# Optimization experiments

Hardware: AMD Instinct MI355X
Metric: run time of the kernel (lower is better)

## Reference

```python
import jax, jax.numpy as jnp
import numpy as np

MASK_VALUE = 0.0  # default `mask=0` scalar in the original forward


def setup_inputs() -> dict:
    key = jax.random.key(0)
    kq, kk, kv = jax.random.split(key, 3)
    b, n, d_k, d_v = 8, 2048, 64, 64
    q = jax.random.normal(kq, (b, n, d_k), dtype=jnp.float32)
    k = jax.random.normal(kk, (b, n, d_k), dtype=jnp.float32)
    v = jax.random.normal(kv, (b, n, d_v), dtype=jnp.float32)
    return {"q": q, "k": k, "v": v}


def reference(q, k, v):
    d_k = q.shape[-1]
    temper = jnp.asarray(d_k, q.dtype) ** 0.5
    # scores: (b, n, n)
    attn = jnp.einsum('bqd,bkd->bqk', q, k) / temper
    # equality-based masking: positions whose score exactly equals the
    # scalar `mask` (default 0) are set to -inf before softmax.
    attn = jnp.where(attn == MASK_VALUE, -jnp.inf, attn)
    # NOTE: the original code calls `attn.masked_fill(look_ahead_mask==0, -inf)`
    # WITHOUT assignment, so the look-ahead mask is a no-op; we omit it faithfully.
    attn = jax.nn.softmax(attn, axis=-1)
    out = jnp.einsum('bqk,bkd->bqd', attn, v)  # (b, n, d_v)
    return out
```

## Files before the change

### kernel.cpp

```cpp
#include <hip/hip_runtime.h>
#include <hip/hip_bf16.h>

typedef __bf16 bf16_t;
typedef bf16_t bf16x2 __attribute__((ext_vector_type(2)));
typedef bf16_t bf16x4 __attribute__((ext_vector_type(4)));
typedef bf16_t bf16x8 __attribute__((ext_vector_type(8)));
typedef float  floatx4  __attribute__((ext_vector_type(4)));
typedef float  floatx16 __attribute__((ext_vector_type(16)));

constexpr int B = 8, N = 2048, D = 64;
constexpr int KSTR = 72;
constexpr int VSTR = 136;
constexpr int TSTR = 65;

__global__ __launch_bounds__(256)
void prepass_kernel(const float* __restrict__ k, const float* __restrict__ v,
                    bf16_t* __restrict__ kb, bf16_t* __restrict__ vt) {
    __shared__ float t[64 * TSTR];
    const int tid = threadIdx.x;
    const int r0  = blockIdx.x * 64;
    const int b   = blockIdx.y;
    if (blockIdx.z == 0) {
        const float* src = k + ((size_t)b * N + r0) * D;
        bf16_t* dst = kb + ((size_t)b * N + r0) * D;
        #pragma unroll
        for (int p = 0; p < 4; ++p) {
            int e = (tid + p * 256) * 4;
            floatx4 f = *(const floatx4*)(src + e);
            bf16x4 o;
            #pragma unroll
            for (int j = 0; j < 4; ++j) o[j] = (bf16_t)f[j];
            *(bf16x4*)(dst + e) = o;
        }
    } else {
        const float* vb = v + ((size_t)b * N + r0) * D;
        #pragma unroll
        for (int p = 0; p < 4; ++p) {
            int e = (tid + p * 256) * 4;
            int row = e >> 6, col = e & 63;
            floatx4 f = *(const floatx4*)(vb + e);
            #pragma unroll
            for (int j = 0; j < 4; ++j) t[(col + j) * TSTR + row] = f[j];
        }
        __syncthreads();
        bf16_t* ob = vt + (size_t)b * D * N + r0;
        #pragma unroll
        for (int p = 0; p < 4; ++p) {
            int e = (tid + p * 256) * 4;
            int drow = e >> 6, kcol = e & 63;
            bf16x4 o;
            #pragma unroll
            for (int j = 0; j < 4; ++j) o[j] = (bf16_t)t[drow * TSTR + kcol + j];
            *(bf16x4*)(ob + (size_t)drow * N + kcol) = o;
        }
    }
}

__global__ __launch_bounds__(256, 4)
void attn_kernel(const float* __restrict__ q, const bf16_t* __restrict__ kb,
                 const bf16_t* __restrict__ vt, float* __restrict__ out) {
    __shared__ bf16_t lds_k[128 * KSTR];
    __shared__ bf16_t lds_v[64 * VSTR];
    __shared__ float  l_buf[3][32];
    float* o_buf = (float*)lds_k;

    const int tid  = threadIdx.x;
    const int lane = tid & 63;
    const int cg   = tid >> 6;
    const int h    = lane >> 5;
    const int l31  = lane & 31;

    const int b  = blockIdx.y;
    const int q0 = blockIdx.x * 32;

    const bf16_t* kbb = kb + (size_t)b * N * D;
    const bf16_t* vbb = vt + (size_t)b * D * N;

    bf16x8 qf[4];
    {
        const float* qp = q + ((size_t)b * N + q0 + l31) * D + h * 8;
        #pragma unroll
        for (int kd = 0; kd < 4; ++kd) {
            floatx4 f0 = *(const floatx4*)(qp + kd * 16);
            floatx4 f1 = *(const floatx4*)(qp + kd * 16 + 4);
            bf16x8 t;
            #pragma unroll
            for (int j = 0; j < 4; ++j) { t[j] = (bf16_t)f0[j]; t[j + 4] = (bf16_t)f1[j]; }
            qf[kd] = t;
        }
    }

    floatx16 o_acc[2];
    #pragma unroll
    for (int d = 0; d < 2; ++d)
        #pragma unroll
        for (int i = 0; i < 16; ++i) o_acc[d][i] = 0.f;
    float l_run = 0.f;

    bf16x8 kreg[4], vreg[4];
    #pragma unroll
    for (int p = 0; p < 4; ++p) {
        int e = (tid + p * 256) * 8;
        kreg[p] = *(const bf16x8*)(kbb + e);
        vreg[p] = *(const bf16x8*)(vbb + (size_t)(e >> 7) * N + (e & 127));
    }

    #pragma unroll 1
    for (int it = 0; it < N / 128; ++it) {
        __syncthreads();
        #pragma unroll
        for (int p = 0; p < 4; ++p) {
            int e = (tid + p * 256) * 8;
            *(bf16x8*)&lds_k[(e >> 6) * KSTR + (e & 63)] = kreg[p];
            *(bf16x8*)&lds_v[(e >> 7) * VSTR + (e & 127)] = vreg[p];
        }
        __syncthreads();
        if (it + 1 < N / 128) {
            const int kv1 = (it + 1) * 128;
            #pragma unroll
            for (int p = 0; p < 4; ++p) {
                int e = (tid + p * 256) * 8;
                kreg[p] = *(const bf16x8*)(kbb + (size_t)kv1 * D + e);
                vreg[p] = *(const bf16x8*)(vbb + (size_t)(e >> 7) * N + kv1 + (e & 127));
            }
        }

        floatx16 s;
        #pragma unroll
        for (int i = 0; i < 16; ++i) s[i] = 0.f;
        #pragma unroll
        for (int kd = 0; kd < 4; ++kd) {
            bf16x8 kf = *(const bf16x8*)&lds_k[(cg * 32 + l31) * KSTR + kd * 16 + h * 8];
            s = __builtin_amdgcn_mfma_f32_32x32x16_bf16(kf, qf[kd], s, 0, 0, 0);
        }

        int q8[8];
        #pragma unroll
        for (int g = 0; g < 8; ++g) {
            union { int i; bf16x2 h2; } u;
            #pragma unroll
            for (int j = 0; j < 2; ++j) {
                float x = s[2 * g + j] * 0.125f;
                float p = (x == 0.0f) ? 0.0f : __expf(x);
                l_run += p;
                u.h2[j] = (bf16_t)p;
            }
            q8[g] = u.i;
        }

        #pragma unroll
        for (int s2 = 0; s2 < 2; ++s2) {
            int r0 = __shfl_xor(q8[4 * s2 + 0], 32);
            int r1 = __shfl_xor(q8[4 * s2 + 1], 32);
            int r2 = __shfl_xor(q8[4 * s2 + 2], 32);
            int r3 = __shfl_xor(q8[4 * s2 + 3], 32);
            union { int i4[4]; bf16x8 v; } bf;
            bf.i4[0] = h ? r2 : q8[4 * s2 + 0];
            bf.i4[1] = h ? r3 : q8[4 * s2 + 1];
            bf.i4[2] = h ? q8[4 * s2 + 2] : r0;
            bf.i4[3] = h ? q8[4 * s2 + 3] : r1;
            #pragma unroll
            for (int dblk = 0; dblk < 2; ++dblk) {
                bf16x8 va = *(const bf16x8*)&lds_v[(dblk * 32 + l31) * VSTR + cg * 32 + s2 * 16 + h * 8];
                o_acc[dblk] = __builtin_amdgcn_mfma_f32_32x32x16_bf16(va, bf.v, o_acc[dblk], 0, 0, 0);
            }
        }
    }

    __syncthreads();

    l_run += __shfl_xor(l_run, 32);

    if (cg > 0) {
        float* ob = o_buf + (size_t)(cg - 1) * 64 * 32;
        #pragma unroll
        for (int dblk = 0; dblk < 2; ++dblk)
            #pragma unroll
            for (int i = 0; i < 16; ++i) {
                const int d = (i & 3) + 8 * (i >> 2) + 4 * h + dblk * 32;
                ob[d * 32 + l31] = o_acc[dblk][i];
            }
        if (h == 0) l_buf[cg - 1][l31] = l_run;
    }
    __syncthreads();
    if (cg == 0) {
        const float inv_l = 1.0f / (l_run + l_buf[0][l31] + l_buf[1][l31] + l_buf[2][l31]);
        float* op = out + ((size_t)b * N + q0 + l31) * D;
        #pragma unroll
        for (int dblk = 0; dblk < 2; ++dblk)
            #pragma unroll
            for (int g = 0; g < 4; ++g) {
                const int d0 = 8 * g + 4 * h + dblk * 32;
                floatx4 o4;
                #pragma unroll
                for (int j = 0; j < 4; ++j) {
                    float sum = o_acc[dblk][4 * g + j];
                    #pragma unroll
                    for (int gg = 0; gg < 3; ++gg)
                        sum += o_buf[(size_t)gg * 64 * 32 + (d0 + j) * 32 + l31];
                    o4[j] = sum * inv_l;
                }
                *(floatx4*)(op + d0) = o4;
            }
    }
}

extern "C" void kernel_launch(void* const* d_in, const int* in_sizes, int n_in,
                              void* d_out, int out_size, void* d_ws, size_t ws_size,
                              hipStream_t stream) {
    const float* q = (const float*)d_in[0];
    const float* k = (const float*)d_in[1];
    const float* v = (const float*)d_in[2];
    float* out = (float*)d_out;
    bf16_t* kb = (bf16_t*)d_ws;
    bf16_t* vt = (bf16_t*)((char*)d_ws + (size_t)B * N * D * 2);

    hipLaunchKernelGGL(prepass_kernel, dim3(N / 64, B, 2), dim3(256), 0, stream, k, v, kb, vt);
    hipLaunchKernelGGL(attn_kernel, dim3(N / 32, B), dim3(256), 0, stream, q, kb, vt, out);
}
```

Measured before the change: 91.22 us.

## Double block to 8 waves with 256-key tiles and XOR-swizzled LDS layout

Each block now runs 512 threads (8 waves) and stages 256 keys per iteration instead of 128, so there are half as many loop iterations and barriers per block. The padded LDS strides are replaced by an XOR swizzle on 16-byte groups to avoid bank conflicts without padding. The final cross-wave reduction now sums 7 partial outputs through a 64KB shared buffer. The larger shared footprint and block size may cut occupancy and lengthen the epilogue reduction.

```diff
diff --git a/kernel.cpp b/kernel.cpp
--- a/kernel.cpp
+++ b/kernel.cpp
@@ -9,8 +9,6 @@
 typedef float  floatx16 __attribute__((ext_vector_type(16)));
 
 constexpr int B = 8, N = 2048, D = 64;
-constexpr int KSTR = 72;
-constexpr int VSTR = 136;
 constexpr int TSTR = 65;
 
 __global__ __launch_bounds__(256)
@@ -56,19 +54,21 @@
     }
 }
 
-__global__ __launch_bounds__(256, 4)
+__global__ __launch_bounds__(512, 4)
 void attn_kernel(const float* __restrict__ q, const bf16_t* __restrict__ kb,
                  const bf16_t* __restrict__ vt, float* __restrict__ out) {
-    __shared__ bf16_t lds_k[128 * KSTR];
-    __shared__ bf16_t lds_v[64 * VSTR];
-    __shared__ float  l_buf[3][32];
-    float* o_buf = (float*)lds_k;
+    __shared__ char smem[65536];
+    bf16_t* lds_k = (bf16_t*)smem;
+    bf16_t* lds_v = (bf16_t*)(smem + 32768);
+    float*  o_buf = (float*)smem;
+    float*  l_buf = (float*)(smem + 57344);
 
     const int tid  = threadIdx.x;
     const int lane = tid & 63;
     const int cg   = tid >> 6;
     const int h    = lane >> 5;
     const int l31  = lane & 31;
+    const int sw   = l31 & 7;
 
     const int b  = blockIdx.y;
     const int q0 = blockIdx.x * 32;
@@ -100,28 +100,30 @@
     bf16x8 kreg[4], vreg[4];
     #pragma unroll
     for (int p = 0; p < 4; ++p) {
-        int e = (tid + p * 256) * 8;
+        int e = (tid + p * 512) * 8;
         kreg[p] = *(const bf16x8*)(kbb + e);
-        vreg[p] = *(const bf16x8*)(vbb + (size_t)(e >> 7) * N + (e & 127));
+        vreg[p] = *(const bf16x8*)(vbb + (size_t)(e >> 8) * N + (e & 255));
     }
 
     #pragma unroll 1
-    for (int it = 0; it < N / 128; ++it) {
+    for (int it = 0; it < N / 256; ++it) {
         __syncthreads();
         #pragma unroll
         for (int p = 0; p < 4; ++p) {
-            int e = (tid + p * 256) * 8;
-            *(bf16x8*)&lds_k[(e >> 6) * KSTR + (e & 63)] = kreg[p];
-            *(bf16x8*)&lds_v[(e >> 7) * VSTR + (e & 127)] = vreg[p];
+            int e  = (tid + p * 512) * 8;
+            int kr = e >> 6, kg = (e >> 3) & 7;
+            *(bf16x8*)&lds_k[kr * 64 + ((kg ^ (kr & 7)) << 3)] = kreg[p];
+            int vr = e >> 8, vg = (e >> 3) & 31;
+            *(bf16x8*)&lds_v[vr * 256 + ((vg ^ (vr & 7)) << 3)] = vreg[p];
         }
         __syncthreads();
-        if (it + 1 < N / 128) {
-            const int kv1 = (it + 1) * 128;
+        if (it + 1 < N / 256) {
+            const int kv1 = (it + 1) * 256;
             #pragma unroll
             for (int p = 0; p < 4; ++p) {
-                int e = (tid + p * 256) * 8;
+                int e = (tid + p * 512) * 8;
                 kreg[p] = *(const bf16x8*)(kbb + (size_t)kv1 * D + e);
-                vreg[p] = *(const bf16x8*)(vbb + (size_t)(e >> 7) * N + kv1 + (e & 127));
+                vreg[p] = *(const bf16x8*)(vbb + (size_t)(e >> 8) * N + kv1 + (e & 255));
             }
         }
 
@@ -130,7 +132,7 @@
         for (int i = 0; i < 16; ++i) s[i] = 0.f;
         #pragma unroll
         for (int kd = 0; kd < 4; ++kd) {
-            bf16x8 kf = *(const bf16x8*)&lds_k[(cg * 32 + l31) * KSTR + kd * 16 + h * 8];
+            bf16x8 kf = *(const bf16x8*)&lds_k[(cg * 32 + l31) * 64 + (((2 * kd + h) ^ sw) << 3)];
             s = __builtin_amdgcn_mfma_f32_32x32x16_bf16(kf, qf[kd], s, 0, 0, 0);
         }
 
@@ -161,7 +163,8 @@
             bf.i4[3] = h ? q8[4 * s2 + 3] : r1;
             #pragma unroll
             for (int dblk = 0; dblk < 2; ++dblk) {
-                bf16x8 va = *(const bf16x8*)&lds_v[(dblk * 32 + l31) * VSTR + cg * 32 + s2 * 16 + h * 8];
+                bf16x8 va = *(const bf16x8*)&lds_v[(dblk * 32 + l31) * 256 +
+                                                   (((cg * 4 + s2 * 2 + h) ^ sw) << 3)];
                 o_acc[dblk] = __builtin_amdgcn_mfma_f32_32x32x16_bf16(va, bf.v, o_acc[dblk], 0, 0, 0);
             }
         }
@@ -180,11 +183,14 @@
                 const int d = (i & 3) + 8 * (i >> 2) + 4 * h + dblk * 32;
                 ob[d * 32 + l31] = o_acc[dblk][i];
             }
-        if (h == 0) l_buf[cg - 1][l31] = l_run;
+        if (h == 0) l_buf[(cg - 1) * 32 + l31] = l_run;
     }
     __syncthreads();
     if (cg == 0) {
-        const float inv_l = 1.0f / (l_run + l_buf[0][l31] + l_buf[1][l31] + l_buf[2][l31]);
+        float lsum = l_run;
+        #pragma unroll
+        for (int gg = 0; gg < 7; ++gg) lsum += l_buf[gg * 32 + l31];
+        const float inv_l = 1.0f / lsum;
         float* op = out + ((size_t)b * N + q0 + l31) * D;
         #pragma unroll
         for (int dblk = 0; dblk < 2; ++dblk)
@@ -196,7 +202,7 @@
                 for (int j = 0; j < 4; ++j) {
                     float sum = o_acc[dblk][4 * g + j];
                     #pragma unroll
-                    for (int gg = 0; gg < 3; ++gg)
+                    for (int gg = 0; gg < 7; ++gg)
                         sum += o_buf[(size_t)gg * 64 * 32 + (d0 + j) * 32 + l31];
                     o4[j] = sum * inv_l;
                 }
@@ -216,5 +222,5 @@
     bf16_t* vt = (bf16_t*)((char*)d_ws + (size_t)B * N * D * 2);
 
     hipLaunchKernelGGL(prepass_kernel, dim3(N / 64, B, 2), dim3(256), 0, stream, k, v, kb, vt);
-    hipLaunchKernelGGL(attn_kernel, dim3(N / 32, B), dim3(256), 0, stream, q, kb, vt, out);
+    hipLaunchKernelGGL(attn_kernel, dim3(N / 32, B), dim3(512), 0, stream, q, kb, vt, out);
 }
```

Result: no change. 91.25 us (+0.0%).
